# Kernel optimization log

Hardware: AMD Instinct MI355X
Metric: run time of the kernel (lower is better)

Reference implementation:

```python
import jax, jax.numpy as jnp
import numpy as np

D1, D2, HIDDEN, BATCH = 8, 8, 256, 131072
SCALE_LIMIT = 1.0


def _mlp(h, w1, b1, w2, b2, w3, b3):
    # Linear-ReLU-Linear-ReLU-Linear, torch Linear convention: y = h @ W.T + b
    h = jax.nn.relu(h @ w1.T + b1)
    h = jax.nn.relu(h @ w2.T + b2)
    return h @ w3.T + b3


def setup_inputs() -> dict:
    key = jax.random.key(0)
    ks = jax.random.split(key, 25)
    inp = {"x": jax.random.normal(ks[0], (BATCH, D1 + D2), dtype=jnp.float32)}
    i = 1
    for net, d_in, d_out in (("s1", D2, D1), ("t1", D2, D1), ("s2", D1, D2), ("t2", D1, D2)):
        for lname, (o, nin) in (("1", (HIDDEN, d_in)), ("2", (HIDDEN, HIDDEN)), ("3", (d_out, HIDDEN))):
            lim = 1.0 / np.sqrt(nin)  # torch default init range
            inp[f"{net}_w{lname}"] = jax.random.uniform(ks[i], (o, nin), jnp.float32, -lim, lim); i += 1
            inp[f"{net}_b{lname}"] = jnp.zeros((o,), jnp.float32)
    return inp


def reference(x,
              s1_w1, s1_b1, s1_w2, s1_b2, s1_w3, s1_b3,
              t1_w1, t1_b1, t1_w2, t1_b2, t1_w3, t1_b3,
              s2_w1, s2_b1, s2_w2, s2_b2, s2_w3, s2_b3,
              t2_w1, t2_b1, t2_w2, t2_b2, t2_w3, t2_b3):
    x1, x2 = x[:, :D1], x[:, D1:]
    # first half-coupling: transform x1 conditioned on x2
    s2 = jnp.tanh(_mlp(x2, s1_w1, s1_b1, s1_w2, s1_b2, s1_w3, s1_b3)) * SCALE_LIMIT
    t2 = _mlp(x2, t1_w1, t1_b1, t1_w2, t1_b2, t1_w3, t1_b3)
    y1 = x1 * jnp.exp(s2) + t2
    # second half-coupling: transform x2 conditioned on y1
    s1 = jnp.tanh(_mlp(y1, s2_w1, s2_b1, s2_w2, s2_b2, s2_w3, s2_b3)) * SCALE_LIMIT
    t1 = _mlp(y1, t2_w1, t2_b1, t2_w2, t2_b2, t2_w3, t2_b3)
    y2 = x2 * jnp.exp(s1) + t1
    y = jnp.concatenate([y1, y2], axis=1)
    log_det = s2.sum(axis=1) + s1.sum(axis=1)
    return y, log_det
```

## Files before the change

### kernel.cpp

```cpp
#include <hip/hip_runtime.h>

#define BATCHN 131072
#define M_TILE 64
#define NTHREADS 1024
#define HPITCH 280
#define W2P_OFF 4096
#define W3P_OFF 73728
#define NET_STRIDE 77824
#define PACK_TOTAL (4 * NET_STRIDE)

typedef _Float16 hv8 __attribute__((ext_vector_type(8)));
typedef _Float16 hv4 __attribute__((ext_vector_type(4)));
typedef __fp16  fp16x2 __attribute__((ext_vector_type(2)));
typedef float f32x16 __attribute__((ext_vector_type(16)));
typedef float f32x4  __attribute__((ext_vector_type(4)));

struct __align__(16) SMEM {
    _Float16 xin[M_TILE][16];
    _Float16 Ha[M_TILE][HPITCH];
    _Float16 Hb[M_TILE][HPITCH];
    float s_tile[M_TILE][8];
    float t_tile[M_TILE][8];
    float ldet[M_TILE];
};

__global__ __launch_bounds__(256) void pack_weights(
    const float* __restrict__ s1w1, const float* __restrict__ s1b1, const float* __restrict__ s1w2, const float* __restrict__ s1b2, const float* __restrict__ s1w3,
    const float* __restrict__ t1w1, const float* __restrict__ t1b1, const float* __restrict__ t1w2, const float* __restrict__ t1b2, const float* __restrict__ t1w3,
    const float* __restrict__ s2w1, const float* __restrict__ s2b1, const float* __restrict__ s2w2, const float* __restrict__ s2b2, const float* __restrict__ s2w3,
    const float* __restrict__ t2w1, const float* __restrict__ t2b1, const float* __restrict__ t2w2, const float* __restrict__ t2b2, const float* __restrict__ t2w3,
    _Float16* __restrict__ wp)
{
    int tid = blockIdx.x * 256 + threadIdx.x;
    if (tid >= PACK_TOTAL) return;
    int net = tid / NET_STRIDE;
    int rem = tid - net * NET_STRIDE;
    const float* w1 = (net == 0) ? s1w1 : (net == 1) ? t1w1 : (net == 2) ? s2w1 : t2w1;
    const float* b1 = (net == 0) ? s1b1 : (net == 1) ? t1b1 : (net == 2) ? s2b1 : t2b1;
    const float* w2 = (net == 0) ? s1w2 : (net == 1) ? t1w2 : (net == 2) ? s2w2 : t2w2;
    const float* b2 = (net == 0) ? s1b2 : (net == 1) ? t1b2 : (net == 2) ? s2b2 : t2b2;
    const float* w3 = (net == 0) ? s1w3 : (net == 1) ? t1w3 : (net == 2) ? s2w3 : t2w3;
    float val;
    if (rem < W2P_OFF) {
        int nt = rem >> 9;
        int l  = (rem >> 3) & 63, j = rem & 7;
        int n  = nt * 32 + (l & 31);
        int k  = ((l >> 5) << 3) + j;
        val = (k < 8) ? w1[n * 8 + k] : (k == 8 ? b1[n] : 0.0f);
    } else if (rem < W3P_OFF) {
        int r = rem - W2P_OFF;
        int chunk = r >> 9;
        int nt = chunk / 17, ks = chunk - nt * 17;
        int l = (r >> 3) & 63, j = r & 7;
        int n = nt * 32 + (l & 31);
        int kk = ((l >> 5) << 3) + j;
        val = (ks < 16) ? w2[n * 256 + ks * 16 + kk] : (kk == 0 ? b2[n] : 0.0f);
    } else {
        int r = rem - W3P_OFF;
        int ks = r >> 9;
        int l = (r >> 3) & 63, j = r & 7;
        int n = l & 15;
        int k = ks * 32 + ((l >> 4) & 3) * 8 + j;
        val = (n < 8) ? w3[n * 256 + k] : 0.0f;
    }
    wp[tid] = (_Float16)val;
}

#define MFMA32(A,B,C) __builtin_amdgcn_mfma_f32_32x32x16_f16((A),(B),(C),0,0,0)

__device__ __forceinline__ void epi4(_Float16* __restrict__ dst, const f32x16& acc)
{
    #pragma unroll
    for (int q = 0; q < 4; ++q) {
        union { hv4 h4; fp16x2 h2[2]; } u;
        u.h2[0] = __builtin_amdgcn_cvt_pkrtz(fmaxf(acc[4*q+0], 0.f), fmaxf(acc[4*q+1], 0.f));
        u.h2[1] = __builtin_amdgcn_cvt_pkrtz(fmaxf(acc[4*q+2], 0.f), fmaxf(acc[4*q+3], 0.f));
        *(hv4*)(dst + 8 * q) = u.h4;
    }
}

__device__ __forceinline__ void layer1(const _Float16* __restrict__ wp, SMEM& sm,
                                       int nt, int mt, int lane, int l31, int hi)
{
    hv8 a = *(const hv8*)(wp + nt * 512 + lane * 8);
    hv8 b = *(const hv8*)(&sm.xin[mt * 32 + l31][hi * 8]);
    f32x16 z = {};
    f32x16 acc = MFMA32(a, b, z);
    epi4(&sm.Ha[mt * 32 + l31][nt * 32 + 4 * hi], acc);
}

__device__ __forceinline__ void layer2(const _Float16* __restrict__ wp, SMEM& sm,
                                       int nt, int mt, int lane, int l31, int hi)
{
    const _Float16* __restrict__ w2 = wp + W2P_OFF + nt * (17 * 512);
    const _Float16* __restrict__ bb = &sm.Ha[mt * 32 + l31][hi * 8];
    f32x16 acc = {};
    #pragma unroll
    for (int ks = 0; ks < 17; ++ks) {
        hv8 a = *(const hv8*)(w2 + ks * 512 + lane * 8);
        hv8 b = *(const hv8*)(bb + ks * 16);
        acc = MFMA32(a, b, acc);
    }
    epi4(&sm.Hb[mt * 32 + l31][nt * 32 + 4 * hi], acc);
}

template <bool IS_S>
__device__ __forceinline__ void layer3(const _Float16* __restrict__ wp, const float* __restrict__ b3,
                                       SMEM& sm, float (*__restrict__ stile)[8],
                                       int wave, int lane)
{
    if (wave >= 4) return;
    const _Float16* __restrict__ w3 = wp + W3P_OFF;
    const int l15 = lane & 15, q = lane >> 4;
    const int m = wave * 16 + l15;
    const _Float16* __restrict__ bb = &sm.Hb[m][q * 8];
    f32x4 acc = {};
    #pragma unroll
    for (int ks = 0; ks < 8; ++ks) {
        hv8 a = *(const hv8*)(w3 + ks * 512 + lane * 8);
        hv8 b = *(const hv8*)(bb + ks * 32);
        acc = __builtin_amdgcn_mfma_f32_16x16x32_f16(a, b, acc, 0, 0, 0);
    }
    if (q < 2) {
        float4 bv = *(const float4*)(b3 + q * 4);
        float o0 = acc[0] + bv.x, o1 = acc[1] + bv.y, o2 = acc[2] + bv.z, o3 = acc[3] + bv.w;
        if (IS_S) { o0 = tanhf(o0); o1 = tanhf(o1); o2 = tanhf(o2); o3 = tanhf(o3); }
        *(float4*)&stile[m][q * 4] = make_float4(o0, o1, o2, o3);
    }
}

__device__ __forceinline__ void stage(const _Float16* __restrict__ wpS, const float* __restrict__ b3S,
                                      const _Float16* __restrict__ wpT, const float* __restrict__ b3T,
                                      SMEM& sm,
                                      int wave, int nt, int mt, int lane, int l31, int hi)
{
    layer1(wpS, sm, nt, mt, lane, l31, hi);
    __syncthreads();
    layer2(wpS, sm, nt, mt, lane, l31, hi);
    __syncthreads();
    layer1(wpT, sm, nt, mt, lane, l31, hi);
    layer3<true >(wpS, b3S, sm, sm.s_tile, wave, lane);
    __syncthreads();
    layer2(wpT, sm, nt, mt, lane, l31, hi);
    __syncthreads();
    layer3<false>(wpT, b3T, sm, sm.t_tile, wave, lane);
    __syncthreads();
}

__global__ __launch_bounds__(NTHREADS, 8) void coupling_kernel(
    const float* __restrict__ x, const _Float16* __restrict__ wp,
    const float* __restrict__ s1b3, const float* __restrict__ t1b3,
    const float* __restrict__ s2b3, const float* __restrict__ t2b3,
    float* __restrict__ out)
{
    __shared__ SMEM sm;
    const int tid  = threadIdx.x;
    const int wave = tid >> 6, lane = tid & 63;
    const int l31  = lane & 31, hi = lane >> 5;
    const int nt   = wave & 7, mt = wave >> 3;
    const long row0 = (long)blockIdx.x * M_TILE;

    {
        int row = tid >> 4, c = tid & 15;
        float v = (c < 8) ? x[(row0 + row) * 16 + 8 + c] : (c == 8 ? 1.0f : 0.0f);
        sm.xin[row][c] = (_Float16)v;
        sm.Ha[row][256 + c] = (c == 0) ? (_Float16)1.0f : (_Float16)0.0f;
    }
    __syncthreads();

    stage(wp + 0 * NET_STRIDE, s1b3, wp + 1 * NET_STRIDE, t1b3, sm, wave, nt, mt, lane, l31, hi);

    if (tid < M_TILE * 8) {
        int row = tid >> 3, c = tid & 7;
        float s = sm.s_tile[row][c];
        float t = sm.t_tile[row][c];
        float x1 = x[(row0 + row) * 16 + c];
        float y = x1 * expf(s) + t;
        out[(row0 + row) * 16 + c] = y;
        sm.xin[row][c] = (_Float16)y;
    }
    if (tid < M_TILE) {
        float a = 0.f;
        #pragma unroll
        for (int c = 0; c < 8; ++c) a += sm.s_tile[tid][c];
        sm.ldet[tid] = a;
    }
    __syncthreads();

    stage(wp + 2 * NET_STRIDE, s2b3, wp + 3 * NET_STRIDE, t2b3, sm, wave, nt, mt, lane, l31, hi);

    if (tid < M_TILE * 8) {
        int row = tid >> 3, c = tid & 7;
        float s = sm.s_tile[row][c];
        float t = sm.t_tile[row][c];
        float x2 = x[(row0 + row) * 16 + 8 + c];
        out[(row0 + row) * 16 + 8 + c] = x2 * expf(s) + t;
    }
    if (tid < M_TILE) {
        float a = sm.ldet[tid];
        #pragma unroll
        for (int c = 0; c < 8; ++c) a += sm.s_tile[tid][c];
        out[(long)BATCHN * 16 + row0 + tid] = a;
    }
}

extern "C" void kernel_launch(void* const* d_in, const int* in_sizes, int n_in,
                              void* d_out, int out_size, void* d_ws, size_t ws_size,
                              hipStream_t stream)
{
    const float* x = (const float*)d_in[0];
    const float* s1w1 = (const float*)d_in[1];  const float* s1b1 = (const float*)d_in[2];
    const float* s1w2 = (const float*)d_in[3];  const float* s1b2 = (const float*)d_in[4];
    const float* s1w3 = (const float*)d_in[5];  const float* s1b3 = (const float*)d_in[6];
    const float* t1w1 = (const float*)d_in[7];  const float* t1b1 = (const float*)d_in[8];
    const float* t1w2 = (const float*)d_in[9];  const float* t1b2 = (const float*)d_in[10];
    const float* t1w3 = (const float*)d_in[11]; const float* t1b3 = (const float*)d_in[12];
    const float* s2w1 = (const float*)d_in[13]; const float* s2b1 = (const float*)d_in[14];
    const float* s2w2 = (const float*)d_in[15]; const float* s2b2 = (const float*)d_in[16];
    const float* s2w3 = (const float*)d_in[17]; const float* s2b3 = (const float*)d_in[18];
    const float* t2w1 = (const float*)d_in[19]; const float* t2b1 = (const float*)d_in[20];
    const float* t2w2 = (const float*)d_in[21]; const float* t2b2 = (const float*)d_in[22];
    const float* t2w3 = (const float*)d_in[23]; const float* t2b3 = (const float*)d_in[24];

    _Float16* wp = (_Float16*)d_ws;

    pack_weights<<<(PACK_TOTAL + 255) / 256, 256, 0, stream>>>(
        s1w1, s1b1, s1w2, s1b2, s1w3,
        t1w1, t1b1, t1w2, t1b2, t1w3,
        s2w1, s2b1, s2w2, s2b2, s2w3,
        t2w1, t2b1, t2w2, t2b2, t2w3, wp);

    coupling_kernel<<<BATCHN / M_TILE, NTHREADS, 0, stream>>>(
        x, wp, s1b3, t1b3, s2b3, t2b3, (float*)d_out);
}
```

Baseline: 215.2 us.

## Double row tile so each wave reuses weight fragments across two M-tiles

Raises the rows per block from 64 to 128 and remaps waves so each wave computes two 32-row MFMA tiles with the same weight fragment. Layer-2 and layer-3 weights are preloaded into registers once and reused. The aim is to halve weight loads from L2 per row and give each wave more MFMA work between loads. In exchange, the block's shared memory roughly doubles, which cuts blocks per CU, and register pressure rises under a lowered launch bound.

```diff
diff --git a/kernel.cpp b/kernel.cpp
--- a/kernel.cpp
+++ b/kernel.cpp
@@ -1,7 +1,7 @@
 #include <hip/hip_runtime.h>
 
 #define BATCHN 131072
-#define M_TILE 64
+#define M_TILE 128
 #define NTHREADS 1024
 #define HPITCH 280
 #define W2P_OFF 4096
@@ -82,26 +82,35 @@
 __device__ __forceinline__ void layer1(const _Float16* __restrict__ wp, SMEM& sm,
                                        int nt, int mt, int lane, int l31, int hi)
 {
-    hv8 a = *(const hv8*)(wp + nt * 512 + lane * 8);
-    hv8 b = *(const hv8*)(&sm.xin[mt * 32 + l31][hi * 8]);
+    hv8 a  = *(const hv8*)(wp + nt * 512 + lane * 8);
+    hv8 b0 = *(const hv8*)(&sm.xin[mt * 64 + l31][hi * 8]);
+    hv8 b1 = *(const hv8*)(&sm.xin[mt * 64 + 32 + l31][hi * 8]);
     f32x16 z = {};
-    f32x16 acc = MFMA32(a, b, z);
-    epi4(&sm.Ha[mt * 32 + l31][nt * 32 + 4 * hi], acc);
+    f32x16 acc0 = MFMA32(a, b0, z);
+    f32x16 acc1 = MFMA32(a, b1, z);
+    epi4(&sm.Ha[mt * 64 + l31][nt * 32 + 4 * hi], acc0);
+    epi4(&sm.Ha[mt * 64 + 32 + l31][nt * 32 + 4 * hi], acc1);
 }
 
 __device__ __forceinline__ void layer2(const _Float16* __restrict__ wp, SMEM& sm,
                                        int nt, int mt, int lane, int l31, int hi)
 {
     const _Float16* __restrict__ w2 = wp + W2P_OFF + nt * (17 * 512);
-    const _Float16* __restrict__ bb = &sm.Ha[mt * 32 + l31][hi * 8];
-    f32x16 acc = {};
+    hv8 w[17];
+    #pragma unroll
+    for (int ks = 0; ks < 17; ++ks) w[ks] = *(const hv8*)(w2 + ks * 512 + lane * 8);
+    const _Float16* __restrict__ bb0 = &sm.Ha[mt * 64 + l31][hi * 8];
+    const _Float16* __restrict__ bb1 = &sm.Ha[mt * 64 + 32 + l31][hi * 8];
+    f32x16 acc0 = {}, acc1 = {};
     #pragma unroll
     for (int ks = 0; ks < 17; ++ks) {
-        hv8 a = *(const hv8*)(w2 + ks * 512 + lane * 8);
-        hv8 b = *(const hv8*)(bb + ks * 16);
-        acc = MFMA32(a, b, acc);
-    }
-    epi4(&sm.Hb[mt * 32 + l31][nt * 32 + 4 * hi], acc);
+        hv8 b0 = *(const hv8*)(bb0 + ks * 16);
+        hv8 b1 = *(const hv8*)(bb1 + ks * 16);
+        acc0 = MFMA32(w[ks], b0, acc0);
+        acc1 = MFMA32(w[ks], b1, acc1);
+    }
+    epi4(&sm.Hb[mt * 64 + l31][nt * 32 + 4 * hi], acc0);
+    epi4(&sm.Hb[mt * 64 + 32 + l31][nt * 32 + 4 * hi], acc1);
 }
 
 template <bool IS_S>
@@ -109,18 +118,18 @@
                                        SMEM& sm, float (*__restrict__ stile)[8],
                                        int wave, int lane)
 {
-    if (wave >= 4) return;
+    if (wave >= 8) return;
     const _Float16* __restrict__ w3 = wp + W3P_OFF;
     const int l15 = lane & 15, q = lane >> 4;
     const int m = wave * 16 + l15;
+    hv8 w[8];
+    #pragma unroll
+    for (int ks = 0; ks < 8; ++ks) w[ks] = *(const hv8*)(w3 + ks * 512 + lane * 8);
     const _Float16* __restrict__ bb = &sm.Hb[m][q * 8];
     f32x4 acc = {};
     #pragma unroll
-    for (int ks = 0; ks < 8; ++ks) {
-        hv8 a = *(const hv8*)(w3 + ks * 512 + lane * 8);
-        hv8 b = *(const hv8*)(bb + ks * 32);
-        acc = __builtin_amdgcn_mfma_f32_16x16x32_f16(a, b, acc, 0, 0, 0);
-    }
+    for (int ks = 0; ks < 8; ++ks)
+        acc = __builtin_amdgcn_mfma_f32_16x16x32_f16(w[ks], *(const hv8*)(bb + ks * 32), acc, 0, 0, 0);
     if (q < 2) {
         float4 bv = *(const float4*)(b3 + q * 4);
         float o0 = acc[0] + bv.x, o1 = acc[1] + bv.y, o2 = acc[2] + bv.z, o3 = acc[3] + bv.w;
@@ -147,7 +156,7 @@
     __syncthreads();
 }
 
-__global__ __launch_bounds__(NTHREADS, 8) void coupling_kernel(
+__global__ __launch_bounds__(NTHREADS, 4) void coupling_kernel(
     const float* __restrict__ x, const _Float16* __restrict__ wp,
     const float* __restrict__ s1b3, const float* __restrict__ t1b3,
     const float* __restrict__ s2b3, const float* __restrict__ t2b3,
@@ -157,11 +166,12 @@
     const int tid  = threadIdx.x;
     const int wave = tid >> 6, lane = tid & 63;
     const int l31  = lane & 31, hi = lane >> 5;
-    const int nt   = wave & 7, mt = wave >> 3;
+    const int mt   = wave & 1, nt = wave >> 1;
     const long row0 = (long)blockIdx.x * M_TILE;
 
-    {
-        int row = tid >> 4, c = tid & 15;
+    #pragma unroll
+    for (int e = tid; e < M_TILE * 16; e += NTHREADS) {
+        int row = e >> 4, c = e & 15;
         float v = (c < 8) ? x[(row0 + row) * 16 + 8 + c] : (c == 8 ? 1.0f : 0.0f);
         sm.xin[row][c] = (_Float16)v;
         sm.Ha[row][256 + c] = (c == 0) ? (_Float16)1.0f : (_Float16)0.0f;
@@ -170,7 +180,7 @@
 
     stage(wp + 0 * NET_STRIDE, s1b3, wp + 1 * NET_STRIDE, t1b3, sm, wave, nt, mt, lane, l31, hi);
 
-    if (tid < M_TILE * 8) {
+    {
         int row = tid >> 3, c = tid & 7;
         float s = sm.s_tile[row][c];
         float t = sm.t_tile[row][c];
@@ -189,7 +199,7 @@
 
     stage(wp + 2 * NET_STRIDE, s2b3, wp + 3 * NET_STRIDE, t2b3, sm, wave, nt, mt, lane, l31, hi);
 
-    if (tid < M_TILE * 8) {
+    {
         int row = tid >> 3, c = tid & 7;
         float s = sm.s_tile[row][c];
         float t = sm.t_tile[row][c];
```

After: 196.1 us. 8.9% less time.
